# Kernel tuning notes

Measured on AMD Instinct MI355X. Metric: run time of the kernel, lower is better.

The kernel has to match this reference:

```python
import jax, jax.numpy as jnp
import numpy as np

B, C = 4096, 1024  # batch_size, label_size (== embedding_dim of dense outputs)


def setup_inputs() -> dict:
    key = jax.random.key(0)
    k1, k2, k3 = jax.random.split(key, 3)
    return {
        "outs": jax.random.normal(k1, (B, C), dtype=jnp.float32),
        "class_centers": jax.random.normal(k2, (C, C), dtype=jnp.float32),
        "batch_label": jax.random.randint(k3, (B,), 0, C, dtype=jnp.int32),
    }


def reference(outs, class_centers, batch_label):
    b, c = outs.shape
    # ---- standard cross-entropy (F.cross_entropy, mean reduction) ----
    logp = jax.nn.log_softmax(outs, axis=-1)
    ce = -jnp.mean(jnp.take_along_axis(logp, batch_label[:, None].astype(jnp.int32), axis=1))

    # ---- InfoNCE with Wasserstein hard-negative mining ----
    # memory bank stores detached embeddings -> centers carry no gradient
    centers = jax.lax.stop_gradient(class_centers)
    pos = centers[batch_label]  # [B, C] positive per anchor

    # calculate_2_wasserstein_dist on 1-D vectors reduces EXACTLY to
    # ||x - y||^2 - 2*d*sqrt(1e-15)  (covariance terms vanish for a single column)
    const = jnp.float32(-2.0 * c * np.sqrt(1e-15))
    x = jax.lax.stop_gradient(outs)  # similarity used only for index selection
    sq = jnp.sum(x * x, axis=-1)  # [B]
    sim = sq[:, None] + sq[None, :] - 2.0 * (x @ x.T) + const  # [B, B]

    # negatives: different label (self automatically excluded: same label)
    mask = batch_label[:, None] != batch_label[None, :]  # [B, B]
    neg_inf = jnp.float32(-1e30)
    # hard negative: largest wasserstein distance among negatives (topk k=1)
    hard_idx = jnp.argmax(jnp.where(mask, sim, neg_inf), axis=1)  # [B]
    # random negative: uniform over negatives via Gumbel-max (torch randperm analogue)
    g = jax.random.gumbel(jax.random.key(42), (b, b), dtype=jnp.float32)
    rand_idx = jnp.argmax(jnp.where(mask, g, neg_inf), axis=1)  # [B]

    pos_sim = jnp.sum(outs * pos, axis=-1)                # [B]
    n_rand = jnp.sum(outs * outs[rand_idx], axis=-1)      # [B]
    n_hard = jnp.sum(outs * outs[hard_idx], axis=-1)      # [B]
    logits = jnp.stack([pos_sim, n_rand, n_hard], axis=1)  # [B, 1+num_negatives]
    info_nce = -jnp.mean(jax.nn.log_softmax(logits, axis=1)[:, 0])

    return ce + 0.1 * info_nce
```

## Files before the change

### kernel.cpp

```cpp
#include <hip/hip_runtime.h>
#include <hip/hip_bf16.h>
#include <stdint.h>

#define Bsz 4096
#define Csz 1024

typedef __attribute__((ext_vector_type(8))) short short8;
typedef __attribute__((ext_vector_type(4))) float f32x4;

__device__ __forceinline__ unsigned fenc(float v) {
  unsigned u = __float_as_uint(v);
  return (u & 0x80000000u) ? ~u : (u | 0x80000000u);
}

__device__ __forceinline__ void load_lds16(const void* g, void* l) {
  __builtin_amdgcn_global_load_lds(
      (const __attribute__((address_space(1))) void*)g,
      (__attribute__((address_space(3))) void*)l, 16, 0, 0);
}

__device__ __forceinline__ uint32_t rotl32(uint32_t x, int r) {
  return (x << r) | (x >> (32 - r));
}

__global__ __launch_bounds__(256) void k_rowstats(
    const float* __restrict__ outs, const int* __restrict__ label,
    unsigned short* __restrict__ xb, float* __restrict__ sq,
    float* __restrict__ ce, unsigned long long* __restrict__ hard,
    int* __restrict__ ridx) {
  const int row = blockIdx.x;
  const int tid = threadIdx.x;
  const int lane = tid & 63, wid = tid >> 6;
  const float4 v = reinterpret_cast<const float4*>(outs + (size_t)row * Csz)[tid];

  ushort4 u4;
  {
    __hip_bfloat16 h;
    h = __float2bfloat16(v.x); u4.x = *reinterpret_cast<const unsigned short*>(&h);
    h = __float2bfloat16(v.y); u4.y = *reinterpret_cast<const unsigned short*>(&h);
    h = __float2bfloat16(v.z); u4.z = *reinterpret_cast<const unsigned short*>(&h);
    h = __float2bfloat16(v.w); u4.w = *reinterpret_cast<const unsigned short*>(&h);
  }
  reinterpret_cast<ushort4*>(xb + (size_t)row * Csz)[tid] = u4;

  __shared__ float wred[3][4];
  float mx = fmaxf(fmaxf(v.x, v.y), fmaxf(v.z, v.w));
#pragma unroll
  for (int off = 32; off; off >>= 1) mx = fmaxf(mx, __shfl_xor(mx, off, 64));
  if (lane == 0) wred[0][wid] = mx;
  __syncthreads();
  mx = fmaxf(fmaxf(wred[0][0], wred[0][1]), fmaxf(wred[0][2], wred[0][3]));

  float se = expf(v.x - mx) + expf(v.y - mx) + expf(v.z - mx) + expf(v.w - mx);
  float s2 = v.x * v.x + v.y * v.y + v.z * v.z + v.w * v.w;
#pragma unroll
  for (int off = 32; off; off >>= 1) {
    se += __shfl_xor(se, off, 64);
    s2 += __shfl_xor(s2, off, 64);
  }
  if (lane == 0) { wred[1][wid] = se; wred[2][wid] = s2; }
  __syncthreads();
  if (tid == 0) {
    const float set = wred[1][0] + wred[1][1] + wred[1][2] + wred[1][3];
    const float sqt = wred[2][0] + wred[2][1] + wred[2][2] + wred[2][3];
    sq[row] = sqt;
    ce[row] = -(outs[(size_t)row * Csz + label[row]] - mx - logf(set));
    hard[row] = 0ull;
  }

  if (row >= 2048) return;

  const int i = row;
  const int li0 = label[i], li1 = label[i + 2048];
  const uint32_t k1c = 42u, k2c = 0x1BD11BDAu ^ 42u;
  unsigned long long b0 = 0ull, b1 = 0ull;
  for (int j = tid; j < Bsz; j += 256) {
    uint32_t x0 = (uint32_t)(i * Bsz + j);
    uint32_t x1 = x0 + 8388608u;
    x1 += k1c;
#define RND(rt) { x0 += x1; x1 = rotl32(x1, rt); x1 ^= x0; }
    RND(13) RND(15) RND(26) RND(6)
    x0 += k1c; x1 += k2c + 1u;
    RND(17) RND(29) RND(16) RND(24)
    x0 += k2c; x1 += 2u;
    RND(13) RND(15) RND(26) RND(6)
    x1 += k1c + 3u;
    RND(17) RND(29) RND(16) RND(24)
    x0 += k1c; x1 += k2c + 4u;
    RND(13) RND(15) RND(26) RND(6)
    x0 += k2c; x1 += 5u;
#undef RND
    const int lj = label[j];
    if (lj != li0) {
      unsigned long long p = (((unsigned long long)(x0 >> 9)) << 32) | (uint32_t)(~j);
      if (p > b0) b0 = p;
    }
    if (lj != li1) {
      unsigned long long p = (((unsigned long long)(x1 >> 9)) << 32) | (uint32_t)(~j);
      if (p > b1) b1 = p;
    }
  }
#pragma unroll
  for (int off = 32; off; off >>= 1) {
    unsigned long long o0 = __shfl_xor(b0, off, 64); if (o0 > b0) b0 = o0;
    unsigned long long o1 = __shfl_xor(b1, off, 64); if (o1 > b1) b1 = o1;
  }
  __shared__ unsigned long long r0[4], r1[4];
  if (lane == 0) { r0[wid] = b0; r1[wid] = b1; }
  __syncthreads();
  if (tid == 0) {
#pragma unroll
    for (int w = 1; w < 4; ++w) {
      if (r0[w] > b0) b0 = r0[w];
      if (r1[w] > b1) b1 = r1[w];
    }
    ridx[i] = (int)(~(uint32_t)b0);
    ridx[i + 2048] = (int)(~(uint32_t)b1);
  }
}

__global__ __launch_bounds__(512, 2) void k_hard(
    const unsigned short* __restrict__ xb, const float* __restrict__ sq,
    const int* __restrict__ label, unsigned long long* __restrict__ hard) {
  __shared__ unsigned short As[2][256 * 64];
  __shared__ unsigned short Bs[2][256 * 64];

  const int bid = (int)blockIdx.x;
  const int swz = (bid & 7) * 32 + (bid >> 3);
  const int bi = swz >> 4, bj = swz & 15;

  const int tid = (int)threadIdx.x;
  const int wid = tid >> 6, lane = tid & 63;
  const int wm = wid >> 2;
  const int wn = wid & 3;
  const int fr = lane & 15;
  const int fq = lane >> 4;
  const int sx = lane & 7;

  f32x4 acc[8][4];
#pragma unroll
  for (int m = 0; m < 8; ++m)
#pragma unroll
    for (int n = 0; n < 4; ++n) acc[m][n] = (f32x4){0.f, 0.f, 0.f, 0.f};

  const unsigned short* Ag = xb + (size_t)(bi * 256) * Csz;
  const unsigned short* Bg = xb + (size_t)(bj * 256) * Csz;
  const int lrow = lane >> 3;
  const int lch = ((lane & 7) ^ lrow) * 8;

  auto STAGE = [&](int buf, int kt) {
#pragma unroll
    for (int c = 0; c < 4; ++c) {
      const int r = wid * 32 + c * 8;
      load_lds16(Ag + (size_t)(r + lrow) * Csz + kt + lch, &As[buf][r * 64]);
      load_lds16(Bg + (size_t)(r + lrow) * Csz + kt + lch, &Bs[buf][r * 64]);
    }
  };
  auto COMPUTE = [&](int buf) {
#pragma unroll
    for (int kh = 0; kh < 2; ++kh) {
      const int choff = ((kh * 4 + fq) ^ sx) * 8;
      short8 a[8], b[4];
#pragma unroll
      for (int m = 0; m < 8; ++m)
        a[m] = *reinterpret_cast<const short8*>(
            &As[buf][(wm * 128 + m * 16 + fr) * 64 + choff]);
#pragma unroll
      for (int n = 0; n < 4; ++n)
        b[n] = *reinterpret_cast<const short8*>(
            &Bs[buf][(wn * 64 + n * 16 + fr) * 64 + choff]);
      __builtin_amdgcn_s_setprio(1);
#pragma unroll
      for (int m = 0; m < 8; ++m)
#pragma unroll
        for (int n = 0; n < 4; ++n)
          acc[m][n] = __builtin_amdgcn_mfma_f32_16x16x32_bf16(a[m], b[n], acc[m][n], 0, 0, 0);
      __builtin_amdgcn_s_setprio(0);
    }
  };

  STAGE(0, 0);
  STAGE(1, 64);
#pragma unroll 1
  for (int t = 0; t < 14; ++t) {
    asm volatile("s_waitcnt vmcnt(8)" ::: "memory");
    __builtin_amdgcn_s_barrier();
    COMPUTE(t & 1);
    asm volatile("s_waitcnt lgkmcnt(0)" ::: "memory");
    __builtin_amdgcn_sched_barrier(0);
    __builtin_amdgcn_s_barrier();
    STAGE(t & 1, (t + 2) * 64);
  }
  asm volatile("s_waitcnt vmcnt(8)" ::: "memory");
  __builtin_amdgcn_s_barrier();
  COMPUTE(0);
  asm volatile("s_waitcnt vmcnt(0)" ::: "memory");
  __builtin_amdgcn_s_barrier();
  COMPUTE(1);

  const float cst = -2.0f * 1024.0f * 3.1622776601683794e-8f;

#pragma unroll
  for (int m = 0; m < 8; ++m) {
#pragma unroll
    for (int r = 0; r < 4; ++r) {
      const int i = bi * 256 + wm * 128 + m * 16 + fq * 4 + r;
      const int li = label[i];
      const float sqi = sq[i];
      float bestv = -3.0e38f;
      int bestj = 0x7FFFFFFF;
#pragma unroll
      for (int n = 0; n < 4; ++n) {
        const int j = bj * 256 + wn * 64 + n * 16 + fr;
        const float val = sqi + sq[j] - 2.0f * acc[m][n][r] + cst;
        if (label[j] != li && val > bestv) { bestv = val; bestj = j; }
      }
      unsigned long long pack =
          (bestj == 0x7FFFFFFF)
              ? 0ull
              : (((unsigned long long)fenc(bestv)) << 32) | (unsigned)(~bestj);
#pragma unroll
      for (int off = 1; off < 16; off <<= 1) {
        unsigned long long o = __shfl_xor(pack, off, 64);
        if (o > pack) pack = o;
      }
      if (fr == 0 && pack) atomicMax(&hard[i], pack);
    }
  }
}

__global__ __launch_bounds__(256) void k_nce(
    const float* __restrict__ outs, const float* __restrict__ centers,
    const int* __restrict__ label, const unsigned long long* __restrict__ hard,
    const int* __restrict__ ridx, float* __restrict__ nce) {
  const int i = blockIdx.x;
  const int tid = threadIdx.x;
  const int lane = tid & 63, wid = tid >> 6;
  const int li = label[i];
  const int jh = (int)(~(uint32_t)hard[i]);
  const int jr = ridx[i];
  const float4 a  = reinterpret_cast<const float4*>(outs + (size_t)i * Csz)[tid];
  const float4 c  = reinterpret_cast<const float4*>(centers + (size_t)li * Csz)[tid];
  const float4 rr = reinterpret_cast<const float4*>(outs + (size_t)jr * Csz)[tid];
  const float4 hh = reinterpret_cast<const float4*>(outs + (size_t)jh * Csz)[tid];
  float dp = a.x * c.x + a.y * c.y + a.z * c.z + a.w * c.w;
  float dr = a.x * rr.x + a.y * rr.y + a.z * rr.z + a.w * rr.w;
  float dh = a.x * hh.x + a.y * hh.y + a.z * hh.z + a.w * hh.w;
#pragma unroll
  for (int off = 32; off; off >>= 1) {
    dp += __shfl_xor(dp, off, 64);
    dr += __shfl_xor(dr, off, 64);
    dh += __shfl_xor(dh, off, 64);
  }
  __shared__ float w0[4], w1[4], w2[4];
  if (lane == 0) { w0[wid] = dp; w1[wid] = dr; w2[wid] = dh; }
  __syncthreads();
  if (tid == 0) {
    const float l0 = w0[0] + w0[1] + w0[2] + w0[3];
    const float l1 = w1[0] + w1[1] + w1[2] + w1[3];
    const float l2 = w2[0] + w2[1] + w2[2] + w2[3];
    const float m = fmaxf(l0, fmaxf(l1, l2));
    const float lse = logf(expf(l0 - m) + expf(l1 - m) + expf(l2 - m));
    nce[i] = -(l0 - m - lse);
  }
}

__global__ __launch_bounds__(1024) void k_final(
    const float* __restrict__ ce, const float* __restrict__ nce,
    float* __restrict__ out) {
  __shared__ double s[1024];
  const int tid = threadIdx.x;
  double v = 0.0;
#pragma unroll
  for (int q = 0; q < 4; ++q) {
    v += (double)ce[tid + q * 1024];
    v += 0.1 * (double)nce[tid + q * 1024];
  }
  s[tid] = v;
  __syncthreads();
  for (int off = 512; off; off >>= 1) {
    if (tid < off) s[tid] += s[tid + off];
    __syncthreads();
  }
  if (tid == 0) out[0] = (float)(s[0] / 4096.0);
}

extern "C" void kernel_launch(void* const* d_in, const int* in_sizes, int n_in,
                              void* d_out, int out_size, void* d_ws, size_t ws_size,
                              hipStream_t stream) {
  const float* outs = (const float*)d_in[0];
  const float* centers = (const float*)d_in[1];
  const int* label = (const int*)d_in[2];
  float* out = (float*)d_out;

  char* ws = (char*)d_ws;
  unsigned short* xb = (unsigned short*)ws;
  unsigned long long* hard = (unsigned long long*)(ws + (8u << 20));
  float* sq = (float*)(ws + (8u << 20) + 32768);
  float* ce = sq + Bsz;
  float* nce = ce + Bsz;
  int* ridx = (int*)(nce + Bsz);

  k_rowstats<<<Bsz, 256, 0, stream>>>(outs, label, xb, sq, ce, hard, ridx);
  k_hard<<<256, 512, 0, stream>>>(xb, sq, label, hard);
  k_nce<<<Bsz, 256, 0, stream>>>(outs, centers, label, hard, ridx, nce);
  k_final<<<1, 1024, 0, stream>>>(ce, nce, out);
}
```

Before: 157.7 us.

## Deepen GEMM pipeline to 4-stage K=32 tiles and fuse final reduction via atomics

The hard-negative GEMM kernel now uses four LDS buffers of K=32 tiles instead of two of K=64, with two loads in flight. A and B staging is interleaved between two half-MFMA phases separated by barriers, so global loads overlap with compute at finer granularity. The separate single-block final reduction kernel is removed. Each row block of the NCE kernel now atomically adds its contribution into a double accumulator, and the last block writes the output. This saves a launch but adds 4096 contended double atomics and extra barriers per K step in the GEMM.

New measurement: 274.6 us. +74.1%, slower.

```diff
diff --git a/kernel.cpp b/kernel.cpp
--- a/kernel.cpp
+++ b/kernel.cpp
@@ -27,11 +27,14 @@
     const float* __restrict__ outs, const int* __restrict__ label,
     unsigned short* __restrict__ xb, float* __restrict__ sq,
     float* __restrict__ ce, unsigned long long* __restrict__ hard,
-    int* __restrict__ ridx) {
+    int* __restrict__ ridx, double* __restrict__ acc,
+    unsigned int* __restrict__ cnt) {
   const int row = blockIdx.x;
   const int tid = threadIdx.x;
   const int lane = tid & 63, wid = tid >> 6;
   const float4 v = reinterpret_cast<const float4*>(outs + (size_t)row * Csz)[tid];
+
+  if (row == 0 && tid == 0) { *acc = 0.0; *cnt = 0u; }
 
   ushort4 u4;
   {
@@ -122,8 +125,8 @@
 __global__ __launch_bounds__(512, 2) void k_hard(
     const unsigned short* __restrict__ xb, const float* __restrict__ sq,
     const int* __restrict__ label, unsigned long long* __restrict__ hard) {
-  __shared__ unsigned short As[2][256 * 64];
-  __shared__ unsigned short Bs[2][256 * 64];
+  __shared__ unsigned short As[4][256 * 32];
+  __shared__ unsigned short Bs[4][256 * 32];
 
   const int bid = (int)blockIdx.x;
   const int swz = (bid & 7) * 32 + (bid >> 3);
@@ -135,7 +138,7 @@
   const int wn = wid & 3;
   const int fr = lane & 15;
   const int fq = lane >> 4;
-  const int sx = lane & 7;
+  const int rsx = fr & 3;
 
   f32x4 acc[8][4];
 #pragma unroll
@@ -145,58 +148,71 @@
 
   const unsigned short* Ag = xb + (size_t)(bi * 256) * Csz;
   const unsigned short* Bg = xb + (size_t)(bj * 256) * Csz;
-  const int lrow = lane >> 3;
-  const int lch = ((lane & 7) ^ lrow) * 8;
-
-  auto STAGE = [&](int buf, int kt) {
-#pragma unroll
-    for (int c = 0; c < 4; ++c) {
-      const int r = wid * 32 + c * 8;
-      load_lds16(Ag + (size_t)(r + lrow) * Csz + kt + lch, &As[buf][r * 64]);
-      load_lds16(Bg + (size_t)(r + lrow) * Csz + kt + lch, &Bs[buf][r * 64]);
-    }
-  };
-  auto COMPUTE = [&](int buf) {
-#pragma unroll
-    for (int kh = 0; kh < 2; ++kh) {
-      const int choff = ((kh * 4 + fq) ^ sx) * 8;
-      short8 a[8], b[4];
-#pragma unroll
-      for (int m = 0; m < 8; ++m)
-        a[m] = *reinterpret_cast<const short8*>(
-            &As[buf][(wm * 128 + m * 16 + fr) * 64 + choff]);
+  const int lrow = lane >> 2;
+  const int lch = ((lane & 3) ^ (lrow & 3)) * 8;
+
+  auto STAGE_A = [&](int t) {
+    const int kt = t * 32;
+    unsigned short* dst = &As[t & 3][0];
+#pragma unroll
+    for (int c = 0; c < 2; ++c) {
+      const int r = wid * 32 + c * 16;
+      load_lds16(Ag + (size_t)(r + lrow) * Csz + kt + lch, dst + r * 32);
+    }
+  };
+  auto STAGE_B = [&](int t) {
+    const int kt = t * 32;
+    unsigned short* dst = &Bs[t & 3][0];
+#pragma unroll
+    for (int c = 0; c < 2; ++c) {
+      const int r = wid * 32 + c * 16;
+      load_lds16(Bg + (size_t)(r + lrow) * Csz + kt + lch, dst + r * 32);
+    }
+  };
+
+  short8 a[4], b[4];
+  auto READ_B = [&](int t) {
+#pragma unroll
+    for (int n = 0; n < 4; ++n)
+      b[n] = *reinterpret_cast<const short8*>(
+          &Bs[t & 3][(wn * 64 + n * 16 + fr) * 32 + ((fq ^ rsx) * 8)]);
+  };
+  auto READ_A4 = [&](int t, int m0) {
+#pragma unroll
+    for (int m = 0; m < 4; ++m)
+      a[m] = *reinterpret_cast<const short8*>(
+          &As[t & 3][(wm * 128 + (m0 + m) * 16 + fr) * 32 + ((fq ^ rsx) * 8)]);
+  };
+  auto MFMA16 = [&](int m0) {
+    __builtin_amdgcn_s_setprio(1);
+#pragma unroll
+    for (int m = 0; m < 4; ++m)
 #pragma unroll
       for (int n = 0; n < 4; ++n)
-        b[n] = *reinterpret_cast<const short8*>(
-            &Bs[buf][(wn * 64 + n * 16 + fr) * 64 + choff]);
-      __builtin_amdgcn_s_setprio(1);
-#pragma unroll
-      for (int m = 0; m < 8; ++m)
-#pragma unroll
-        for (int n = 0; n < 4; ++n)
-          acc[m][n] = __builtin_amdgcn_mfma_f32_16x16x32_bf16(a[m], b[n], acc[m][n], 0, 0, 0);
-      __builtin_amdgcn_s_setprio(0);
-    }
-  };
-
-  STAGE(0, 0);
-  STAGE(1, 64);
+        acc[m0 + m][n] =
+            __builtin_amdgcn_mfma_f32_16x16x32_bf16(a[m], b[n], acc[m0 + m][n], 0, 0, 0);
+    __builtin_amdgcn_s_setprio(0);
+  };
+
+  STAGE_A(0); STAGE_B(0); STAGE_A(1); STAGE_B(1);
+
 #pragma unroll 1
-  for (int t = 0; t < 14; ++t) {
-    asm volatile("s_waitcnt vmcnt(8)" ::: "memory");
-    __builtin_amdgcn_s_barrier();
-    COMPUTE(t & 1);
-    asm volatile("s_waitcnt lgkmcnt(0)" ::: "memory");
+  for (int t = 0; t < 32; ++t) {
+    if (t < 31) asm volatile("s_waitcnt vmcnt(4) lgkmcnt(0)" ::: "memory");
+    else        asm volatile("s_waitcnt vmcnt(0) lgkmcnt(0)" ::: "memory");
     __builtin_amdgcn_sched_barrier(0);
     __builtin_amdgcn_s_barrier();
-    STAGE(t & 1, (t + 2) * 64);
-  }
-  asm volatile("s_waitcnt vmcnt(8)" ::: "memory");
-  __builtin_amdgcn_s_barrier();
-  COMPUTE(0);
-  asm volatile("s_waitcnt vmcnt(0)" ::: "memory");
-  __builtin_amdgcn_s_barrier();
-  COMPUTE(1);
+    READ_B(t);
+    READ_A4(t, 0);
+    if (t < 30) STAGE_A(t + 2);
+    __builtin_amdgcn_s_barrier();
+    MFMA16(0);
+    __builtin_amdgcn_s_barrier();
+    READ_A4(t, 4);
+    if (t < 30) STAGE_B(t + 2);
+    __builtin_amdgcn_s_barrier();
+    MFMA16(4);
+  }
 
   const float cst = -2.0f * 1024.0f * 3.1622776601683794e-8f;
 
@@ -229,23 +245,25 @@
   }
 }
 
-__global__ __launch_bounds__(256) void k_nce(
+__global__ __launch_bounds__(256) void k_ncefin(
     const float* __restrict__ outs, const float* __restrict__ centers,
     const int* __restrict__ label, const unsigned long long* __restrict__ hard,
-    const int* __restrict__ ridx, float* __restrict__ nce) {
+    const int* __restrict__ ridx, const float* __restrict__ ce,
+    double* __restrict__ acc, unsigned int* __restrict__ cnt,
+    float* __restrict__ out) {
   const int i = blockIdx.x;
   const int tid = threadIdx.x;
   const int lane = tid & 63, wid = tid >> 6;
   const int li = label[i];
   const int jh = (int)(~(uint32_t)hard[i]);
   const int jr = ridx[i];
-  const float4 a  = reinterpret_cast<const float4*>(outs + (size_t)i * Csz)[tid];
-  const float4 c  = reinterpret_cast<const float4*>(centers + (size_t)li * Csz)[tid];
+  const float4 aa = reinterpret_cast<const float4*>(outs + (size_t)i * Csz)[tid];
+  const float4 cc = reinterpret_cast<const float4*>(centers + (size_t)li * Csz)[tid];
   const float4 rr = reinterpret_cast<const float4*>(outs + (size_t)jr * Csz)[tid];
   const float4 hh = reinterpret_cast<const float4*>(outs + (size_t)jh * Csz)[tid];
-  float dp = a.x * c.x + a.y * c.y + a.z * c.z + a.w * c.w;
-  float dr = a.x * rr.x + a.y * rr.y + a.z * rr.z + a.w * rr.w;
-  float dh = a.x * hh.x + a.y * hh.y + a.z * hh.z + a.w * hh.w;
+  float dp = aa.x * cc.x + aa.y * cc.y + aa.z * cc.z + aa.w * cc.w;
+  float dr = aa.x * rr.x + aa.y * rr.y + aa.z * rr.z + aa.w * rr.w;
+  float dh = aa.x * hh.x + aa.y * hh.y + aa.z * hh.z + aa.w * hh.w;
 #pragma unroll
   for (int off = 32; off; off >>= 1) {
     dp += __shfl_xor(dp, off, 64);
@@ -261,28 +279,14 @@
     const float l2 = w2[0] + w2[1] + w2[2] + w2[3];
     const float m = fmaxf(l0, fmaxf(l1, l2));
     const float lse = logf(expf(l0 - m) + expf(l1 - m) + expf(l2 - m));
-    nce[i] = -(l0 - m - lse);
-  }
-}
-
-__global__ __launch_bounds__(1024) void k_final(
-    const float* __restrict__ ce, const float* __restrict__ nce,
-    float* __restrict__ out) {
-  __shared__ double s[1024];
-  const int tid = threadIdx.x;
-  double v = 0.0;
-#pragma unroll
-  for (int q = 0; q < 4; ++q) {
-    v += (double)ce[tid + q * 1024];
-    v += 0.1 * (double)nce[tid + q * 1024];
-  }
-  s[tid] = v;
-  __syncthreads();
-  for (int off = 512; off; off >>= 1) {
-    if (tid < off) s[tid] += s[tid + off];
-    __syncthreads();
-  }
-  if (tid == 0) out[0] = (float)(s[0] / 4096.0);
+    const float nce_i = -(l0 - m - lse);
+    atomicAdd(acc, (double)ce[i] + 0.1 * (double)nce_i);
+    __threadfence();
+    if (atomicAdd(cnt, 1u) == (unsigned)(Bsz - 1)) {
+      const double s = atomicAdd(acc, 0.0);
+      out[0] = (float)(s / (double)Bsz);
+    }
+  }
 }
 
 extern "C" void kernel_launch(void* const* d_in, const int* in_sizes, int n_in,
@@ -298,11 +302,11 @@
   unsigned long long* hard = (unsigned long long*)(ws + (8u << 20));
   float* sq = (float*)(ws + (8u << 20) + 32768);
   float* ce = sq + Bsz;
-  float* nce = ce + Bsz;
-  int* ridx = (int*)(nce + Bsz);
-
-  k_rowstats<<<Bsz, 256, 0, stream>>>(outs, label, xb, sq, ce, hard, ridx);
+  int* ridx = (int*)(ce + Bsz);
+  double* acc = (double*)(ridx + Bsz);
+  unsigned int* cnt = (unsigned int*)(acc + 1);
+
+  k_rowstats<<<Bsz, 256, 0, stream>>>(outs, label, xb, sq, ce, hard, ridx, acc, cnt);
   k_hard<<<256, 512, 0, stream>>>(xb, sq, label, hard);
-  k_nce<<<Bsz, 256, 0, stream>>>(outs, centers, label, hard, ridx, nce);
-  k_final<<<1, 1024, 0, stream>>>(ce, nce, out);
-}
+  k_ncefin<<<Bsz, 256, 0, stream>>>(outs, centers, label, hard, ridx, ce, acc, cnt, out);
+}
```

## Split bf16 GEMM main loop into 8-phase ping-pong schedule with interleaved staging

Applied to the files above, without the earlier changes.

Restructures the k_hard GEMM main loop from a coarse compute-then-stage pattern into eight phases per 128-wide k step. Each phase loads a quarter of the fragments from LDS, issues a slice of the next global-to-LDS copies, then runs 16 MFMAs between barriers. The aim is to overlap global loads, LDS reads and MFMA work more finely and keep the matrix cores busy. In exchange it adds many more barriers per iteration and more fragile vmcnt bookkeeping.

After: 158.1 us. About the same (+0.3%).

```diff
diff --git a/kernel.cpp b/kernel.cpp
--- a/kernel.cpp
+++ b/kernel.cpp
@@ -135,7 +135,6 @@
   const int wn = wid & 3;
   const int fr = lane & 15;
   const int fq = lane >> 4;
-  const int sx = lane & 7;
 
   f32x4 acc[8][4];
 #pragma unroll
@@ -148,55 +147,71 @@
   const int lrow = lane >> 3;
   const int lch = ((lane & 7) ^ lrow) * 8;
 
-  auto STAGE = [&](int buf, int kt) {
-#pragma unroll
-    for (int c = 0; c < 4; ++c) {
-      const int r = wid * 32 + c * 8;
-      load_lds16(Ag + (size_t)(r + lrow) * Csz + kt + lch, &As[buf][r * 64]);
-      load_lds16(Bg + (size_t)(r + lrow) * Csz + kt + lch, &Bs[buf][r * 64]);
-    }
-  };
-  auto COMPUTE = [&](int buf) {
-#pragma unroll
-    for (int kh = 0; kh < 2; ++kh) {
-      const int choff = ((kh * 4 + fq) ^ sx) * 8;
-      short8 a[8], b[4];
-#pragma unroll
-      for (int m = 0; m < 8; ++m)
-        a[m] = *reinterpret_cast<const short8*>(
-            &As[buf][(wm * 128 + m * 16 + fr) * 64 + choff]);
-#pragma unroll
-      for (int n = 0; n < 4; ++n)
-        b[n] = *reinterpret_cast<const short8*>(
-            &Bs[buf][(wn * 64 + n * 16 + fr) * 64 + choff]);
-      __builtin_amdgcn_s_setprio(1);
-#pragma unroll
-      for (int m = 0; m < 8; ++m)
-#pragma unroll
-        for (int n = 0; n < 4; ++n)
-          acc[m][n] = __builtin_amdgcn_mfma_f32_16x16x32_bf16(a[m], b[n], acc[m][n], 0, 0, 0);
-      __builtin_amdgcn_s_setprio(0);
-    }
-  };
-
-  STAGE(0, 0);
-  STAGE(1, 64);
+#define STAGE_A_MH(b, kt, mh) { \
+    const int rb0 = (mh) * 64 + wid * 8; \
+    load_lds16(Ag + (size_t)(rb0 + lrow) * Csz + (kt) + lch, &As[b][rb0 * 64]); \
+    const int rb1 = 128 + (mh) * 64 + wid * 8; \
+    load_lds16(Ag + (size_t)(rb1 + lrow) * Csz + (kt) + lch, &As[b][rb1 * 64]); }
+#define STAGE_B_P(b, kt, p) { \
+    const int rb0 = (p) * 128 + wid * 8; \
+    load_lds16(Bg + (size_t)(rb0 + lrow) * Csz + (kt) + lch, &Bs[b][rb0 * 64]); \
+    const int rb1 = (p) * 128 + 64 + wid * 8; \
+    load_lds16(Bg + (size_t)(rb1 + lrow) * Csz + (kt) + lch, &Bs[b][rb1 * 64]); }
+
+#define VMSYNC(NSTR) { \
+    asm volatile("s_waitcnt vmcnt(" NSTR ")" ::: "memory"); \
+    __builtin_amdgcn_sched_barrier(0); \
+    __builtin_amdgcn_s_barrier(); }
+
+#define PHASE(bbuf, kh, mh, STAGE_STMT) { \
+    short8 af[4], bf[4]; \
+    const int co = (((kh) * 4 + fq) ^ (fr & 7)) * 8; \
+    _Pragma("unroll") \
+    for (int m = 0; m < 4; ++m) \
+      af[m] = *reinterpret_cast<const short8*>( \
+          &As[bbuf][(wm * 128 + (mh) * 64 + m * 16 + fr) * 64 + co]); \
+    _Pragma("unroll") \
+    for (int n = 0; n < 4; ++n) \
+      bf[n] = *reinterpret_cast<const short8*>( \
+          &Bs[bbuf][(wn * 64 + n * 16 + fr) * 64 + co]); \
+    STAGE_STMT; \
+    __builtin_amdgcn_s_barrier(); \
+    asm volatile("s_waitcnt lgkmcnt(0)" ::: "memory"); \
+    __builtin_amdgcn_sched_barrier(0); \
+    __builtin_amdgcn_s_setprio(1); \
+    _Pragma("unroll") \
+    for (int m = 0; m < 4; ++m) \
+      _Pragma("unroll") \
+      for (int n = 0; n < 4; ++n) \
+        acc[(mh) * 4 + m][n] = __builtin_amdgcn_mfma_f32_16x16x32_bf16( \
+            af[m], bf[n], acc[(mh) * 4 + m][n], 0, 0, 0); \
+    __builtin_amdgcn_s_setprio(0); \
+    __builtin_amdgcn_s_barrier(); }
+
+  STAGE_A_MH(0, 0, 0); STAGE_A_MH(0, 0, 1);
+  STAGE_B_P(0, 0, 0);  STAGE_B_P(0, 0, 1);
+  STAGE_A_MH(1, 64, 0);
+
 #pragma unroll 1
-  for (int t = 0; t < 14; ++t) {
-    asm volatile("s_waitcnt vmcnt(8)" ::: "memory");
-    __builtin_amdgcn_s_barrier();
-    COMPUTE(t & 1);
-    asm volatile("s_waitcnt lgkmcnt(0)" ::: "memory");
-    __builtin_amdgcn_sched_barrier(0);
-    __builtin_amdgcn_s_barrier();
-    STAGE(t & 1, (t + 2) * 64);
-  }
-  asm volatile("s_waitcnt vmcnt(8)" ::: "memory");
-  __builtin_amdgcn_s_barrier();
-  COMPUTE(0);
-  asm volatile("s_waitcnt vmcnt(0)" ::: "memory");
-  __builtin_amdgcn_s_barrier();
-  COMPUTE(1);
+  for (int j = 0; j < 8; ++j) {
+    const int ktB = j * 128 + 64;
+    const int ktC = j * 128 + 128;
+    const int ktD = j * 128 + 192;
+    VMSYNC("2");
+    PHASE(0, 0, 0, STAGE_A_MH(1, ktB, 1));
+    PHASE(0, 0, 1, STAGE_B_P(1, ktB, 0));
+    PHASE(0, 1, 0, STAGE_B_P(1, ktB, 1));
+    PHASE(0, 1, 1, if (j < 7) STAGE_A_MH(0, ktC, 0));
+    if (j < 7) { VMSYNC("2"); } else { VMSYNC("0"); }
+    PHASE(1, 0, 0, if (j < 7) STAGE_A_MH(0, ktC, 1));
+    PHASE(1, 0, 1, if (j < 7) STAGE_B_P(0, ktC, 0));
+    PHASE(1, 1, 0, if (j < 7) STAGE_B_P(0, ktC, 1));
+    PHASE(1, 1, 1, if (j < 7) STAGE_A_MH(1, ktD, 0));
+  }
+#undef PHASE
+#undef VMSYNC
+#undef STAGE_A_MH
+#undef STAGE_B_P
 
   const float cst = -2.0f * 1024.0f * 3.1622776601683794e-8f;
 
```
